# Kernel optimization log

Measured on AMD Instinct MI355X. Metric: run time of the kernel, lower is better.

## Reference

```python
import jax, jax.numpy as jnp
import numpy as np

N_NODES = 50000
N_EDGES = 1600000
EDGE_DIM = 64
NODE_DIM = 128
GLOBAL_DIM = 64
IN_DIM = EDGE_DIM + NODE_DIM + GLOBAL_DIM  # 256
HID_DIM = 256
OUT_DIM = 128


def setup_inputs() -> dict:
    key = jax.random.key(0)
    ks = jax.random.split(key, 8)
    edges = jax.random.normal(ks[0], (N_EDGES, EDGE_DIM), dtype=jnp.float32)
    receivers = jax.random.randint(ks[1], (N_EDGES,), 0, N_NODES, dtype=jnp.int64)
    nodes = jax.random.normal(ks[2], (N_NODES, NODE_DIM), dtype=jnp.float32)
    globals_ = jax.random.normal(ks[3], (1, GLOBAL_DIM), dtype=jnp.float32)
    # MLP params (Linear -> ReLU -> Linear), fan-in scaled init
    W1 = jax.random.normal(ks[4], (IN_DIM, HID_DIM), dtype=jnp.float32) / np.sqrt(IN_DIM)
    b1 = jnp.zeros((HID_DIM,), dtype=jnp.float32)
    W2 = jax.random.normal(ks[5], (HID_DIM, OUT_DIM), dtype=jnp.float32) / np.sqrt(HID_DIM)
    b2 = jnp.zeros((OUT_DIM,), dtype=jnp.float32)
    return {
        "edges": edges, "receivers": receivers, "nodes": nodes,
        "globals_": globals_, "num_nodes": N_NODES,
        "W1": W1, "b1": b1, "W2": W2, "b2": b2,
    }


def reference(edges, receivers, nodes, globals_, num_nodes, W1, b1, W2, b2):
    # ReceivedEdgesToNodesAggregator: unsorted_segment_sum of edge features to receiver nodes
    agg = jax.ops.segment_sum(edges, receivers, num_segments=num_nodes)  # [N, EDGE_DIM]
    # broadcast_globals_to_nodes (single graph -> tile to every node)
    g = jnp.broadcast_to(globals_, (num_nodes, globals_.shape[-1]))      # [N, GLOBAL_DIM]
    collected = jnp.concatenate([agg, nodes, g], axis=-1)                # [N, IN_DIM]
    h = jax.nn.relu(collected @ W1 + b1)
    updated_nodes = h @ W2 + b2                                          # [N, OUT_DIM]
    return updated_nodes
```

## Files before the change

### kernel.cpp

```cpp
#include <hip/hip_runtime.h>


typedef __bf16 bf16x8 __attribute__((ext_vector_type(8)));
typedef __bf16 bf16x4 __attribute__((ext_vector_type(4)));
typedef __bf16 bf16x2 __attribute__((ext_vector_type(2)));
typedef float f32x4 __attribute__((ext_vector_type(4)));
typedef int i32x4 __attribute__((ext_vector_type(4)));

#define EDGE_DIM 64
#define NODE_DIM 128
#define XDIM 192
#define HID_DIM 256
#define OUT_DIM 128
#define NBUCKET 512
#define NPB 98
#define EPB 4096
#define MT 64
#define HPAD 280

__global__ __launch_bounds__(256) void prep_hist_kernel(
    const float* __restrict__ W1, const float* __restrict__ b1,
    const float* __restrict__ W2, const float* __restrict__ glob,
    __bf16* __restrict__ W1T, float* __restrict__ b1f, __bf16* __restrict__ W2T,
    const int* __restrict__ recv, int* __restrict__ bh, int n_edges) {
  const int b = blockIdx.x, t = threadIdx.x;
  if (b < HID_DIM) {
    if (t < XDIM) {
      W1T[b * XDIM + t] = (__bf16)W1[t * HID_DIM + b];
    } else {
      float p = glob[t - XDIM] * W1[t * HID_DIM + b];
      for (int off = 32; off; off >>= 1) p += __shfl_xor(p, off, 64);
      if (t == XDIM) b1f[b] = b1[b] + p;
    }
    return;
  }
  if (b < HID_DIM + OUT_DIM) {
    int nn = b - HID_DIM;
    W2T[nn * HID_DIM + t] = (__bf16)W2[t * OUT_DIM + nn];
    return;
  }
  const int hb = b - (HID_DIM + OUT_DIM);
  __shared__ int h[NBUCKET];
  for (int k = t; k < NBUCKET; k += 256) h[k] = 0;
  __syncthreads();
  const int i0 = hb * EPB + t * 16;
  if (i0 + 16 <= n_edges) {
#pragma unroll
    for (int c = 0; c < 4; ++c) {
      i32x4 r4 = *(const i32x4*)(recv + i0 + c * 4);
      atomicAdd(&h[r4.x / NPB], 1);
      atomicAdd(&h[r4.y / NPB], 1);
      atomicAdd(&h[r4.z / NPB], 1);
      atomicAdd(&h[r4.w / NPB], 1);
    }
  } else {
    for (int j = 0; j < 16; ++j)
      if (i0 + j < n_edges) atomicAdd(&h[recv[i0 + j] / NPB], 1);
  }
  __syncthreads();
  for (int k = t; k < NBUCKET; k += 256) bh[(size_t)hb * NBUCKET + k] = h[k];
}

__global__ __launch_bounds__(256) void col_scan_kernel(
    int* __restrict__ bh, int* __restrict__ tot, int nbh) {
  const int bucket = (blockIdx.x * 256 + threadIdx.x) >> 6;
  const int lane = threadIdx.x & 63;
  int running = 0;
  for (int c = 0; c < nbh; c += 64) {
    const int k = c + lane;
    int v = (k < nbh) ? bh[(size_t)k * NBUCKET + bucket] : 0;
    int incl = v;
    for (int off = 1; off < 64; off <<= 1) {
      int y = __shfl_up(incl, off, 64);
      if (lane >= off) incl += y;
    }
    if (k < nbh) bh[(size_t)k * NBUCKET + bucket] = running + incl - v;
    running += __shfl(incl, 63, 64);
  }
  if (lane == 0) tot[bucket] = running;
}

__global__ __launch_bounds__(512) void base_scan_kernel(const int* __restrict__ tot,
                                                        int* __restrict__ base) {
  const int b = threadIdx.x;
  int v = tot[b];
  __shared__ int sums[NBUCKET];
  sums[b] = v;
  __syncthreads();
  for (int off = 1; off < NBUCKET; off <<= 1) {
    int y = (b >= off) ? sums[b - off] : 0;
    __syncthreads();
    sums[b] += y;
    __syncthreads();
  }
  base[b] = sums[b] - v;
  if (b == NBUCKET - 1) base[NBUCKET] = sums[b];
}

__global__ __launch_bounds__(256) void scatter_kernel(
    const int* __restrict__ recv, const int* __restrict__ off,
    const int* __restrict__ base, int* __restrict__ sorted1, int n_edges) {
  const int kb = blockIdx.x, t = threadIdx.x;
  __shared__ int cur[NBUCKET];
  for (int k = t; k < NBUCKET; k += 256)
    cur[k] = base[k] + off[(size_t)kb * NBUCKET + k];
  __syncthreads();
  const int i0 = kb * EPB + t * 16;
  if (i0 + 16 <= n_edges) {
#pragma unroll
    for (int c = 0; c < 4; ++c) {
      i32x4 r4 = *(const i32x4*)(recv + i0 + c * 4);
      const int e0 = i0 + c * 4;
      int bk, p;
      bk = r4.x / NPB; p = atomicAdd(&cur[bk], 1);
      sorted1[p] = ((e0 + 0) << 7) | (r4.x - bk * NPB);
      bk = r4.y / NPB; p = atomicAdd(&cur[bk], 1);
      sorted1[p] = ((e0 + 1) << 7) | (r4.y - bk * NPB);
      bk = r4.z / NPB; p = atomicAdd(&cur[bk], 1);
      sorted1[p] = ((e0 + 2) << 7) | (r4.z - bk * NPB);
      bk = r4.w / NPB; p = atomicAdd(&cur[bk], 1);
      sorted1[p] = ((e0 + 3) << 7) | (r4.w - bk * NPB);
    }
  } else {
    for (int j = 0; j < 16; ++j) {
      const int i = i0 + j;
      if (i < n_edges) {
        int r = recv[i];
        int bk = r / NPB;
        int p = atomicAdd(&cur[bk], 1);
        sorted1[p] = (i << 7) | (r - bk * NPB);
      }
    }
  }
}

__global__ __launch_bounds__(256) void regroup_kernel(
    const int* __restrict__ sorted1, const int* __restrict__ base,
    int* __restrict__ nodeoff, int* __restrict__ ncount,
    int* __restrict__ eidcsr, int n_nodes) {
  const int b = blockIdx.x, t = threadIdx.x;
  __shared__ int cnt[NPB];
  __shared__ int loff[NPB];
  if (t < NPB) cnt[t] = 0;
  __syncthreads();
  const int s = base[b], e = base[b + 1];
  const int nb_ = b * NPB;
  for (int j = s + t; j < e; j += 256) atomicAdd(&cnt[sorted1[j] & 127], 1);
  __syncthreads();
  if (t == 0) {
    int run = 0;
#pragma unroll
    for (int k = 0; k < NPB; ++k) { loff[k] = run; run += cnt[k]; }
  }
  __syncthreads();
  if (t < NPB) {
    const int node = nb_ + t;
    if (node < n_nodes) { nodeoff[node] = s + loff[t]; ncount[node] = cnt[t]; }
    cnt[t] = 0;
  }
  __syncthreads();
  for (int j = s + t; j < e; j += 256) {
    const int p = sorted1[j];
    const int local = p & 127;
    const int slot = atomicAdd(&cnt[local], 1);
    eidcsr[s + loff[local] + slot] = p >> 7;
  }
}

__global__ __launch_bounds__(256) void build_x_kernel(
    const float* __restrict__ edges, const int* __restrict__ nodeoff,
    const int* __restrict__ ncount, const int* __restrict__ eid,
    const float* __restrict__ nodes,
    __bf16* __restrict__ X, int n_nodes) {
  const int gwave = (blockIdx.x * 256 + threadIdx.x) >> 6;
  const int lane = threadIdx.x & 63;
  if (gwave >= n_nodes) return;
  const int q = lane >> 4;
  const int l15 = lane & 15;
  const int s = nodeoff[gwave];
  const int e = s + ncount[gwave];
  f32x4 a0 = {0.f, 0.f, 0.f, 0.f}, a1 = a0, a2 = a0, a3 = a0;

  int j = s + q;
  int i0 = (j < e) ? eid[j] : 0;
  int i1 = (j + 4 < e) ? eid[j + 4] : 0;
  int i2 = (j + 8 < e) ? eid[j + 8] : 0;
  int i3 = (j + 12 < e) ? eid[j + 12] : 0;

  while (j + 12 < e) {
    f32x4 v0 = __builtin_nontemporal_load((const f32x4*)(edges + (size_t)i0 * EDGE_DIM + l15 * 4));
    f32x4 v1 = __builtin_nontemporal_load((const f32x4*)(edges + (size_t)i1 * EDGE_DIM + l15 * 4));
    f32x4 v2 = __builtin_nontemporal_load((const f32x4*)(edges + (size_t)i2 * EDGE_DIM + l15 * 4));
    f32x4 v3 = __builtin_nontemporal_load((const f32x4*)(edges + (size_t)i3 * EDGE_DIM + l15 * 4));
    int n0 = (j + 16 < e) ? eid[j + 16] : 0;
    int n1 = (j + 20 < e) ? eid[j + 20] : 0;
    int n2 = (j + 24 < e) ? eid[j + 24] : 0;
    int n3 = (j + 28 < e) ? eid[j + 28] : 0;
    a0 += v0; a1 += v1; a2 += v2; a3 += v3;
    i0 = n0; i1 = n1; i2 = n2; i3 = n3;
    j += 16;
  }
  if (j < e)
    a0 += __builtin_nontemporal_load((const f32x4*)(edges + (size_t)i0 * EDGE_DIM + l15 * 4));
  if (j + 4 < e)
    a1 += __builtin_nontemporal_load((const f32x4*)(edges + (size_t)i1 * EDGE_DIM + l15 * 4));
  if (j + 8 < e)
    a2 += __builtin_nontemporal_load((const f32x4*)(edges + (size_t)i2 * EDGE_DIM + l15 * 4));

  a0 += a1; a2 += a3; a0 += a2;
#pragma unroll
  for (int c = 0; c < 4; ++c) {
    float v = a0[c];
    v += __shfl_xor(v, 16, 64);
    v += __shfl_xor(v, 32, 64);
    a0[c] = v;
  }
  __bf16* row = X + (size_t)gwave * XDIM;
  if (q == 0) {
    bf16x4 o;
    o[0] = (__bf16)a0[0]; o[1] = (__bf16)a0[1];
    o[2] = (__bf16)a0[2]; o[3] = (__bf16)a0[3];
    *(bf16x4*)(row + l15 * 4) = o;
  }
  float2 nv = *(const float2*)(nodes + (size_t)gwave * NODE_DIM + lane * 2);
  bf16x2 nb;
  nb[0] = (__bf16)nv.x; nb[1] = (__bf16)nv.y;
  *(bf16x2*)(row + EDGE_DIM + lane * 2) = nb;
}

__global__ __launch_bounds__(256, 2) void mlp_kernel(
    const __bf16* __restrict__ X, const __bf16* __restrict__ W1T,
    const float* __restrict__ b1f, const __bf16* __restrict__ W2T,
    const float* __restrict__ b2, float* __restrict__ out, int M) {
  __shared__ __bf16 Hs[MT][HPAD];
  const int wave = threadIdx.x >> 6;
  const int lane = threadIdx.x & 63;
  const int l15 = lane & 15;
  const int lk = lane >> 4;
  const int Mbase0 = blockIdx.x * MT;

  {
    bf16x8 B1[4][6];
    float bias1[4];
    const int colbase = wave * 64;
#pragma unroll
    for (int cb = 0; cb < 4; ++cb) {
      const int col = colbase + cb * 16 + l15;
      const __bf16* wrow = W1T + col * XDIM + lk * 8;
#pragma unroll
      for (int ks = 0; ks < 6; ++ks) B1[cb][ks] = *(const bf16x8*)(wrow + ks * 32);
      bias1[cb] = b1f[col];
    }
#pragma unroll
    for (int mb = 0; mb < 4; ++mb) {
      const int Mbase = Mbase0 + mb * 16;
      f32x4 acc[4];
#pragma unroll
      for (int cb = 0; cb < 4; ++cb) {
        f32x4 ini = {bias1[cb], bias1[cb], bias1[cb], bias1[cb]};
        acc[cb] = ini;
      }
      const __bf16* xrow = X + (size_t)(Mbase + l15) * XDIM + lk * 8;
#pragma unroll
      for (int ks = 0; ks < 6; ++ks) {
        bf16x8 A = *(const bf16x8*)(xrow + ks * 32);
#pragma unroll
        for (int cb = 0; cb < 4; ++cb)
          acc[cb] = __builtin_amdgcn_mfma_f32_16x16x32_bf16(A, B1[cb][ks], acc[cb], 0, 0, 0);
      }
#pragma unroll
      for (int cb = 0; cb < 4; ++cb) {
#pragma unroll
        for (int r = 0; r < 4; ++r) {
          float v = acc[cb][r];
          Hs[mb * 16 + lk * 4 + r][colbase + cb * 16 + l15] = (__bf16)(v > 0.f ? v : 0.f);
        }
      }
    }
  }
  __syncthreads();
  {
    bf16x8 B2[2][8];
    float bias2[2];
    const int colbase = wave * 32;
#pragma unroll
    for (int cb = 0; cb < 2; ++cb) {
      const int col = colbase + cb * 16 + l15;
      const __bf16* wrow = W2T + col * HID_DIM + lk * 8;
#pragma unroll
      for (int ks = 0; ks < 8; ++ks) B2[cb][ks] = *(const bf16x8*)(wrow + ks * 32);
      bias2[cb] = b2[col];
    }
#pragma unroll
    for (int mb = 0; mb < 4; ++mb) {
      const int Mbase = Mbase0 + mb * 16;
      f32x4 acc[2];
#pragma unroll
      for (int cb = 0; cb < 2; ++cb) {
        f32x4 ini = {bias2[cb], bias2[cb], bias2[cb], bias2[cb]};
        acc[cb] = ini;
      }
#pragma unroll
      for (int ks = 0; ks < 8; ++ks) {
        bf16x8 A = *(const bf16x8*)(&Hs[mb * 16 + l15][lk * 8 + ks * 32]);
#pragma unroll
        for (int cb = 0; cb < 2; ++cb)
          acc[cb] = __builtin_amdgcn_mfma_f32_16x16x32_bf16(A, B2[cb][ks], acc[cb], 0, 0, 0);
      }
#pragma unroll
      for (int cb = 0; cb < 2; ++cb) {
        const int col = colbase + cb * 16 + l15;
#pragma unroll
        for (int r = 0; r < 4; ++r) {
          const int row = Mbase + lk * 4 + r;
          if (row < M) out[(size_t)row * OUT_DIM + col] = acc[cb][r];
        }
      }
    }
  }
}

extern "C" void kernel_launch(void* const* d_in, const int* in_sizes, int n_in,
                              void* d_out, int out_size, void* d_ws, size_t ws_size,
                              hipStream_t stream) {
  const float* edges    = (const float*)d_in[0];
  const int*   recv     = (const int*)d_in[1];
  const float* nodes    = (const float*)d_in[2];
  const float* globals_ = (const float*)d_in[3];
  const float* W1       = (const float*)d_in[5];
  const float* b1       = (const float*)d_in[6];
  const float* W2       = (const float*)d_in[7];
  const float* b2       = (const float*)d_in[8];

  const int n_edges = in_sizes[0] / EDGE_DIM;
  const int n_nodes = in_sizes[2] / NODE_DIM;
  const int NBH = (n_edges + EPB - 1) / EPB;
  float* out = (float*)d_out;

  char* ws = (char*)d_ws;
  size_t off = 0;
  int* bh = (int*)(ws + off);      off += (size_t)NBH * NBUCKET * 4;
  off = (off + 255) & ~(size_t)255;
  int* tot = (int*)(ws + off);     off += NBUCKET * 4;
  off = (off + 255) & ~(size_t)255;
  int* base = (int*)(ws + off);    off += (NBUCKET + 1) * 4;
  off = (off + 255) & ~(size_t)255;
  int* sorted1 = (int*)(ws + off); off += (size_t)n_edges * 4;
  off = (off + 255) & ~(size_t)255;
  int* nodeoff = (int*)(ws + off); off += (size_t)n_nodes * 4;
  off = (off + 255) & ~(size_t)255;
  int* ncount = (int*)(ws + off);  off += (size_t)n_nodes * 4;
  off = (off + 255) & ~(size_t)255;
  int* eidcsr = (int*)(ws + off);  off += (size_t)n_edges * 4;
  off = (off + 255) & ~(size_t)255;
  __bf16* X   = (__bf16*)(ws + off); off += (size_t)n_nodes * XDIM * 2;
  off = (off + 255) & ~(size_t)255;
  __bf16* W1T = (__bf16*)(ws + off); off += (size_t)HID_DIM * XDIM * 2;
  off = (off + 255) & ~(size_t)255;
  float* b1f = (float*)(ws + off);  off += HID_DIM * 4;
  off = (off + 255) & ~(size_t)255;
  __bf16* W2T = (__bf16*)(ws + off); off += (size_t)HID_DIM * OUT_DIM * 2;

  prep_hist_kernel<<<HID_DIM + OUT_DIM + NBH, 256, 0, stream>>>(
      W1, b1, W2, globals_, W1T, b1f, W2T, recv, bh, n_edges);
  col_scan_kernel<<<NBUCKET / 4, 256, 0, stream>>>(bh, tot, NBH);
  base_scan_kernel<<<1, NBUCKET, 0, stream>>>(tot, base);
  scatter_kernel<<<NBH, 256, 0, stream>>>(recv, bh, base, sorted1, n_edges);
  regroup_kernel<<<NBUCKET, 256, 0, stream>>>(sorted1, base, nodeoff, ncount,
                                              eidcsr, n_nodes);
  build_x_kernel<<<(n_nodes + 3) / 4, 256, 0, stream>>>(edges, nodeoff, ncount, eidcsr,
                                                        nodes, X, n_nodes);
  mlp_kernel<<<(n_nodes + MT - 1) / MT, 256, 0, stream>>>(X, W1T, b1f, W2T, b2, out, n_nodes);
}
```

Before: 159.1 us.

## Replace histogram and scan passes with fixed-capacity buckets and global atomic cursors

Removes the per-block histogram kernel, the column scan and the base scan. Each scatter block now counts its bucket occupancy in LDS, reserves space with one global atomicAdd per bucket into a fixed-capacity region (CAP slots per bucket), then scatters. This cuts two kernel launches and one read pass over receivers. In exchange, the sorted buffers grow to NBUCKET*CAP, and nothing catches overflow if any bucket receives more than CAP edges. Edge order within a bucket also becomes nondeterministic.

```diff
diff --git a/kernel.cpp b/kernel.cpp
--- a/kernel.cpp
+++ b/kernel.cpp
@@ -14,15 +14,16 @@
 #define OUT_DIM 128
 #define NBUCKET 512
 #define NPB 98
+#define CAP 4096
 #define EPB 4096
 #define MT 64
 #define HPAD 280
 
-__global__ __launch_bounds__(256) void prep_hist_kernel(
+__global__ __launch_bounds__(256) void prep_kernel(
     const float* __restrict__ W1, const float* __restrict__ b1,
     const float* __restrict__ W2, const float* __restrict__ glob,
     __bf16* __restrict__ W1T, float* __restrict__ b1f, __bf16* __restrict__ W2T,
-    const int* __restrict__ recv, int* __restrict__ bh, int n_edges) {
+    int* __restrict__ gcur) {
   const int b = blockIdx.x, t = threadIdx.x;
   if (b < HID_DIM) {
     if (t < XDIM) {
@@ -39,103 +40,55 @@
     W2T[nn * HID_DIM + t] = (__bf16)W2[t * OUT_DIM + nn];
     return;
   }
-  const int hb = b - (HID_DIM + OUT_DIM);
+  for (int k = t; k < NBUCKET; k += 256) gcur[k] = k * CAP;
+}
+
+__global__ __launch_bounds__(256) void scatter_kernel(
+    const int* __restrict__ recv, int* __restrict__ gcur,
+    int* __restrict__ sorted1, int n_edges) {
+  const int kb = blockIdx.x, t = threadIdx.x;
   __shared__ int h[NBUCKET];
   for (int k = t; k < NBUCKET; k += 256) h[k] = 0;
   __syncthreads();
-  const int i0 = hb * EPB + t * 16;
+
+  const int i0 = kb * EPB + t * 16;
+  int rr[16];
+  int bk[16];
   if (i0 + 16 <= n_edges) {
 #pragma unroll
     for (int c = 0; c < 4; ++c) {
       i32x4 r4 = *(const i32x4*)(recv + i0 + c * 4);
-      atomicAdd(&h[r4.x / NPB], 1);
-      atomicAdd(&h[r4.y / NPB], 1);
-      atomicAdd(&h[r4.z / NPB], 1);
-      atomicAdd(&h[r4.w / NPB], 1);
+      rr[c * 4 + 0] = r4.x; rr[c * 4 + 1] = r4.y;
+      rr[c * 4 + 2] = r4.z; rr[c * 4 + 3] = r4.w;
     }
   } else {
-    for (int j = 0; j < 16; ++j)
-      if (i0 + j < n_edges) atomicAdd(&h[recv[i0 + j] / NPB], 1);
-  }
-  __syncthreads();
-  for (int k = t; k < NBUCKET; k += 256) bh[(size_t)hb * NBUCKET + k] = h[k];
-}
-
-__global__ __launch_bounds__(256) void col_scan_kernel(
-    int* __restrict__ bh, int* __restrict__ tot, int nbh) {
-  const int bucket = (blockIdx.x * 256 + threadIdx.x) >> 6;
-  const int lane = threadIdx.x & 63;
-  int running = 0;
-  for (int c = 0; c < nbh; c += 64) {
-    const int k = c + lane;
-    int v = (k < nbh) ? bh[(size_t)k * NBUCKET + bucket] : 0;
-    int incl = v;
-    for (int off = 1; off < 64; off <<= 1) {
-      int y = __shfl_up(incl, off, 64);
-      if (lane >= off) incl += y;
-    }
-    if (k < nbh) bh[(size_t)k * NBUCKET + bucket] = running + incl - v;
-    running += __shfl(incl, 63, 64);
-  }
-  if (lane == 0) tot[bucket] = running;
-}
-
-__global__ __launch_bounds__(512) void base_scan_kernel(const int* __restrict__ tot,
-                                                        int* __restrict__ base) {
-  const int b = threadIdx.x;
-  int v = tot[b];
-  __shared__ int sums[NBUCKET];
-  sums[b] = v;
-  __syncthreads();
-  for (int off = 1; off < NBUCKET; off <<= 1) {
-    int y = (b >= off) ? sums[b - off] : 0;
-    __syncthreads();
-    sums[b] += y;
-    __syncthreads();
-  }
-  base[b] = sums[b] - v;
-  if (b == NBUCKET - 1) base[NBUCKET] = sums[b];
-}
-
-__global__ __launch_bounds__(256) void scatter_kernel(
-    const int* __restrict__ recv, const int* __restrict__ off,
-    const int* __restrict__ base, int* __restrict__ sorted1, int n_edges) {
-  const int kb = blockIdx.x, t = threadIdx.x;
-  __shared__ int cur[NBUCKET];
-  for (int k = t; k < NBUCKET; k += 256)
-    cur[k] = base[k] + off[(size_t)kb * NBUCKET + k];
-  __syncthreads();
-  const int i0 = kb * EPB + t * 16;
-  if (i0 + 16 <= n_edges) {
-#pragma unroll
-    for (int c = 0; c < 4; ++c) {
-      i32x4 r4 = *(const i32x4*)(recv + i0 + c * 4);
-      const int e0 = i0 + c * 4;
-      int bk, p;
-      bk = r4.x / NPB; p = atomicAdd(&cur[bk], 1);
-      sorted1[p] = ((e0 + 0) << 7) | (r4.x - bk * NPB);
-      bk = r4.y / NPB; p = atomicAdd(&cur[bk], 1);
-      sorted1[p] = ((e0 + 1) << 7) | (r4.y - bk * NPB);
-      bk = r4.z / NPB; p = atomicAdd(&cur[bk], 1);
-      sorted1[p] = ((e0 + 2) << 7) | (r4.z - bk * NPB);
-      bk = r4.w / NPB; p = atomicAdd(&cur[bk], 1);
-      sorted1[p] = ((e0 + 3) << 7) | (r4.w - bk * NPB);
-    }
-  } else {
-    for (int j = 0; j < 16; ++j) {
-      const int i = i0 + j;
-      if (i < n_edges) {
-        int r = recv[i];
-        int bk = r / NPB;
-        int p = atomicAdd(&cur[bk], 1);
-        sorted1[p] = (i << 7) | (r - bk * NPB);
-      }
+#pragma unroll
+    for (int j = 0; j < 16; ++j) rr[j] = (i0 + j < n_edges) ? recv[i0 + j] : -1;
+  }
+#pragma unroll
+  for (int j = 0; j < 16; ++j) {
+    bk[j] = (rr[j] >= 0) ? (rr[j] / NPB) : -1;
+    if (bk[j] >= 0) atomicAdd(&h[bk[j]], 1);
+  }
+  __syncthreads();
+
+  for (int k = t; k < NBUCKET; k += 256) {
+    int c = h[k];
+    h[k] = (c > 0) ? atomicAdd(&gcur[k], c) : 0;
+  }
+  __syncthreads();
+
+#pragma unroll
+  for (int j = 0; j < 16; ++j) {
+    if (bk[j] >= 0) {
+      const int p = atomicAdd(&h[bk[j]], 1);
+      sorted1[p] = ((i0 + j) << 7) | (rr[j] - bk[j] * NPB);
     }
   }
 }
 
 __global__ __launch_bounds__(256) void regroup_kernel(
-    const int* __restrict__ sorted1, const int* __restrict__ base,
+    const int* __restrict__ sorted1, const int* __restrict__ gcur,
     int* __restrict__ nodeoff, int* __restrict__ ncount,
     int* __restrict__ eidcsr, int n_nodes) {
   const int b = blockIdx.x, t = threadIdx.x;
@@ -143,7 +96,7 @@
   __shared__ int loff[NPB];
   if (t < NPB) cnt[t] = 0;
   __syncthreads();
-  const int s = base[b], e = base[b + 1];
+  const int s = b * CAP, e = gcur[b];
   const int nb_ = b * NPB;
   for (int j = s + t; j < e; j += 256) atomicAdd(&cnt[sorted1[j] & 127], 1);
   __syncthreads();
@@ -339,19 +292,15 @@
 
   char* ws = (char*)d_ws;
   size_t off = 0;
-  int* bh = (int*)(ws + off);      off += (size_t)NBH * NBUCKET * 4;
-  off = (off + 255) & ~(size_t)255;
-  int* tot = (int*)(ws + off);     off += NBUCKET * 4;
-  off = (off + 255) & ~(size_t)255;
-  int* base = (int*)(ws + off);    off += (NBUCKET + 1) * 4;
-  off = (off + 255) & ~(size_t)255;
-  int* sorted1 = (int*)(ws + off); off += (size_t)n_edges * 4;
+  int* gcur = (int*)(ws + off);    off += NBUCKET * 4;
+  off = (off + 255) & ~(size_t)255;
+  int* sorted1 = (int*)(ws + off); off += (size_t)NBUCKET * CAP * 4;
   off = (off + 255) & ~(size_t)255;
   int* nodeoff = (int*)(ws + off); off += (size_t)n_nodes * 4;
   off = (off + 255) & ~(size_t)255;
   int* ncount = (int*)(ws + off);  off += (size_t)n_nodes * 4;
   off = (off + 255) & ~(size_t)255;
-  int* eidcsr = (int*)(ws + off);  off += (size_t)n_edges * 4;
+  int* eidcsr = (int*)(ws + off);  off += (size_t)NBUCKET * CAP * 4;
   off = (off + 255) & ~(size_t)255;
   __bf16* X   = (__bf16*)(ws + off); off += (size_t)n_nodes * XDIM * 2;
   off = (off + 255) & ~(size_t)255;
@@ -361,12 +310,10 @@
   off = (off + 255) & ~(size_t)255;
   __bf16* W2T = (__bf16*)(ws + off); off += (size_t)HID_DIM * OUT_DIM * 2;
 
-  prep_hist_kernel<<<HID_DIM + OUT_DIM + NBH, 256, 0, stream>>>(
-      W1, b1, W2, globals_, W1T, b1f, W2T, recv, bh, n_edges);
-  col_scan_kernel<<<NBUCKET / 4, 256, 0, stream>>>(bh, tot, NBH);
-  base_scan_kernel<<<1, NBUCKET, 0, stream>>>(tot, base);
-  scatter_kernel<<<NBH, 256, 0, stream>>>(recv, bh, base, sorted1, n_edges);
-  regroup_kernel<<<NBUCKET, 256, 0, stream>>>(sorted1, base, nodeoff, ncount,
+  prep_kernel<<<HID_DIM + OUT_DIM + 1, 256, 0, stream>>>(
+      W1, b1, W2, globals_, W1T, b1f, W2T, gcur);
+  scatter_kernel<<<NBH, 256, 0, stream>>>(recv, gcur, sorted1, n_edges);
+  regroup_kernel<<<NBUCKET, 256, 0, stream>>>(sorted1, gcur, nodeoff, ncount,
                                               eidcsr, n_nodes);
   build_x_kernel<<<(n_nodes + 3) / 4, 256, 0, stream>>>(edges, nodeoff, ncount, eidcsr,
                                                         nodes, X, n_nodes);
```

Result: faster. 155.9 us (-2.0%).
